# Optimization experiments

Hardware: AMD Instinct MI355X
Metric: run time of the kernel (lower is better)

## Reference

```python
import jax, jax.numpy as jnp
import numpy as np

LEAKY_SLOPE = 0.2   # LeakyReLU alpha from __init__
MASK_VAL = -9.0e15  # same sentinel as torch reference


def setup_inputs() -> dict:
    key = jax.random.key(0)
    k1, k2, k3 = jax.random.split(key, 3)
    B, N, D = 512, 64, 128
    hidden = jax.random.normal(k1, (B, N, D), dtype=jnp.float32)
    adj = jax.random.randint(k2, (B, N, N), 0, 5)  # edge types 0..4
    a = jax.random.normal(k3, (4, D), dtype=jnp.float32) * 0.1  # stacked a_0..a_3
    return {"hidden": hidden, "adj": adj, "a": a}


def reference(hidden, adj, a):
    # e_k[b,i,j] = leakyrelu( sum_d hidden[b,i,d]*hidden[b,j,d]*a[k,d] )
    # Never materializes the [B,N,N,D] tensor: contract (hidden * a_k) @ hidden^T.
    e = jnp.einsum('kd,bid,bjd->kbij', a, hidden, hidden)  # [4,B,N,N]
    e = jnp.where(e >= 0, e, LEAKY_SLOPE * e)
    mask = jnp.full(e.shape[1:], MASK_VAL, dtype=e.dtype)
    alpha = jnp.where(adj == 1, e[0], mask)
    alpha = jnp.where(adj == 2, e[1], alpha)
    alpha = jnp.where(adj == 3, e[2], alpha)
    alpha = jnp.where(adj == 4, e[3], alpha)
    alpha = jax.nn.softmax(alpha, axis=-1)          # [B,N,N]
    return jnp.matmul(alpha, hidden)                # [B,N,D]
```

## Files before the change

### kernel.cpp

```cpp
#include <hip/hip_runtime.h>
#include <hip/hip_bf16.h>


#define NB 512
#define NN 64
#define ND 128
#define HS 136
#define AS 72
#define AJS 65

typedef __bf16 bf16x8 __attribute__((ext_vector_type(8)));
typedef __bf16 bf16x4 __attribute__((ext_vector_type(4)));
typedef float  f32x4  __attribute__((ext_vector_type(4)));

__global__ __launch_bounds__(256)
void gat_kernel(const float* __restrict__ hidden,
                const int*   __restrict__ adj,
                const float* __restrict__ a,
                float*       __restrict__ out)
{
    __shared__ __bf16 h_lds[NN * HS];
    __shared__ __bf16 h_tr[8 * NN * 16];
    __shared__ __bf16 al_lds[NN * AS];
    __shared__ float  a_lds[4 * ND];
    __shared__ int    adj_lds[NN * AJS];

    const int t = threadIdx.x;
    const int l = t & 63;
    const int w = t >> 6;
    const int b = blockIdx.x;
    const int g  = l >> 4;
    const int g8 = g << 3;
    const int i0 = w * 16 + (g << 2);

    const float4* hin = (const float4*)(hidden + (size_t)b * NN * ND);
    #pragma unroll
    for (int it = 0; it < 8; ++it) {
        int row = ((l >> 2) & 15) | ((it >> 1) << 4);
        int f4  = (l & 3) | (w << 2) | ((it & 1) << 4);
        float4 v = hin[row * 32 + f4];
        bf16x4 pk = { (__bf16)v.x, (__bf16)v.y, (__bf16)v.z, (__bf16)v.w };
        int c4 = f4 << 2;
        *(bf16x4*)&h_lds[row * HS + c4] = pk;
        *(bf16x4*)&h_tr[((c4 >> 4) << 10) + (row << 4) + (c4 & 15)] = pk;
    }
    const int4* adjin = (const int4*)(adj + (size_t)b * NN * NN);
    #pragma unroll
    for (int it = 0; it < 4; ++it) {
        int idx = it * 256 + t;
        int4 v = adjin[idx];
        int ri = idx >> 4;
        int c4 = (idx & 15) << 2;
        int* p = &adj_lds[ri * AJS + c4];
        p[0] = v.x; p[1] = v.y; p[2] = v.z; p[3] = v.w;
    }
    a_lds[t]       = a[t];
    a_lds[t + 256] = a[t + 256];
    __syncthreads();

    const int irow = w * 16 + (l & 15);
    f32x4 acc[4][4];
    #pragma unroll
    for (int ct = 0; ct < 4; ++ct)
        #pragma unroll
        for (int k = 0; k < 4; ++k)
            acc[ct][k] = (f32x4){0.f, 0.f, 0.f, 0.f};

    #pragma unroll
    for (int kk = 0; kk < 4; ++kk) {
        int d0 = kk * 32 + g8;
        bf16x8 hf = *(const bf16x8*)&h_lds[irow * HS + d0];
        float hff[8];
        #pragma unroll
        for (int e = 0; e < 8; ++e) hff[e] = (float)hf[e];
        bf16x8 hk[4];
        #pragma unroll
        for (int k = 0; k < 4; ++k) {
            float4 alo = *(const float4*)&a_lds[k * ND + d0];
            float4 ahi = *(const float4*)&a_lds[k * ND + d0 + 4];
            bf16x8 r;
            r[0] = (__bf16)(hff[0] * alo.x); r[1] = (__bf16)(hff[1] * alo.y);
            r[2] = (__bf16)(hff[2] * alo.z); r[3] = (__bf16)(hff[3] * alo.w);
            r[4] = (__bf16)(hff[4] * ahi.x); r[5] = (__bf16)(hff[5] * ahi.y);
            r[6] = (__bf16)(hff[6] * ahi.z); r[7] = (__bf16)(hff[7] * ahi.w);
            hk[k] = r;
        }
        bf16x8 bfr[4];
        #pragma unroll
        for (int ct = 0; ct < 4; ++ct)
            bfr[ct] = *(const bf16x8*)&h_lds[(ct * 16 + (l & 15)) * HS + d0];
        #pragma unroll
        for (int ct = 0; ct < 4; ++ct)
            #pragma unroll
            for (int k = 0; k < 4; ++k)
                acc[ct][k] = __builtin_amdgcn_mfma_f32_16x16x32_bf16(hk[k], bfr[ct], acc[ct][k], 0, 0, 0);
    }

    float sel[4][4];
    #pragma unroll
    for (int ct = 0; ct < 4; ++ct)
        #pragma unroll
        for (int r = 0; r < 4; ++r) {
            int av = adj_lds[(i0 + r) * AJS + ct * 16 + (l & 15)];
            float e0 = fmaxf(acc[ct][0][r], 0.2f * acc[ct][0][r]);
            float e1 = fmaxf(acc[ct][1][r], 0.2f * acc[ct][1][r]);
            float e2 = fmaxf(acc[ct][2][r], 0.2f * acc[ct][2][r]);
            float e3 = fmaxf(acc[ct][3][r], 0.2f * acc[ct][3][r]);
            sel[ct][r] = av == 1 ? e0 : av == 2 ? e1 : av == 3 ? e2 : av == 4 ? e3 : -9.0e15f;
        }

    #pragma unroll
    for (int r = 0; r < 4; ++r) {
        float m = fmaxf(fmaxf(sel[0][r], sel[1][r]), fmaxf(sel[2][r], sel[3][r]));
        m = fmaxf(m, __shfl_xor(m, 1));
        m = fmaxf(m, __shfl_xor(m, 2));
        m = fmaxf(m, __shfl_xor(m, 4));
        m = fmaxf(m, __shfl_xor(m, 8));
        float p0 = __expf(sel[0][r] - m);
        float p1 = __expf(sel[1][r] - m);
        float p2 = __expf(sel[2][r] - m);
        float p3 = __expf(sel[3][r] - m);
        float s = p0 + p1 + p2 + p3;
        s += __shfl_xor(s, 1);
        s += __shfl_xor(s, 2);
        s += __shfl_xor(s, 4);
        s += __shfl_xor(s, 8);
        float inv = 1.0f / s;
        int i = i0 + r;
        al_lds[i * AS +  0 + (l & 15)] = (__bf16)(p0 * inv);
        al_lds[i * AS + 16 + (l & 15)] = (__bf16)(p1 * inv);
        al_lds[i * AS + 32 + (l & 15)] = (__bf16)(p2 * inv);
        al_lds[i * AS + 48 + (l & 15)] = (__bf16)(p3 * inv);
    }

    const int ia = w * 16 + (l & 15);
    bf16x8 pB0 = *(const bf16x8*)&al_lds[ia * AS + g8];
    bf16x8 pB1 = *(const bf16x8*)&al_lds[ia * AS + 32 + g8];
    float* outb = out + (size_t)b * NN * ND;
    unsigned trb = (unsigned)(unsigned long long)(&h_tr[0])
                 + (unsigned)(((l & 15) << 3) + (g << 8));
    #pragma unroll
    for (int dt = 0; dt < 8; ++dt) {
        unsigned ab = trb + dt * 2048;
        bf16x4 r0, r1, r2, r3;
        asm volatile("ds_read_b64_tr_b16 %0, %1"             : "=v"(r0) : "v"(ab));
        asm volatile("ds_read_b64_tr_b16 %0, %1 offset:128"  : "=v"(r1) : "v"(ab));
        asm volatile("ds_read_b64_tr_b16 %0, %1 offset:1024" : "=v"(r2) : "v"(ab));
        asm volatile("ds_read_b64_tr_b16 %0, %1 offset:1152" : "=v"(r3) : "v"(ab));
        asm volatile("s_waitcnt lgkmcnt(0)" ::: "memory");
        __builtin_amdgcn_sched_barrier(0);
        bf16x8 A0 = __builtin_shufflevector(r0, r1, 0, 1, 2, 3, 4, 5, 6, 7);
        bf16x8 A1 = __builtin_shufflevector(r2, r3, 0, 1, 2, 3, 4, 5, 6, 7);
        f32x4 o = {0.f, 0.f, 0.f, 0.f};
        o = __builtin_amdgcn_mfma_f32_16x16x32_bf16(A0, pB0, o, 0, 0, 0);
        o = __builtin_amdgcn_mfma_f32_16x16x32_bf16(A1, pB1, o, 0, 0, 0);
        float4 st = { o[0], o[1], o[2], o[3] };
        *(float4*)&outb[ia * ND + dt * 16 + (g << 2)] = st;
    }
}

extern "C" void kernel_launch(void* const* d_in, const int* in_sizes, int n_in,
                              void* d_out, int out_size, void* d_ws, size_t ws_size,
                              hipStream_t stream) {
    const float* hidden = (const float*)d_in[0];
    const int*   adj    = (const int*)d_in[1];
    const float* a      = (const float*)d_in[2];
    float*       out    = (float*)d_out;
    gat_kernel<<<NB, 256, 0, stream>>>(hidden, adj, a, out);
}
```

Before: 17.12 us.

## Process two batches per block with warp-specialized score/softmax and PV pipeline

Each 512-thread block now handles two batch items. Warps 0-3 compute scores and softmax while warps 4-7 stage the second batch's hidden tile and then run the alpha·V product for the first batch, so the two stages overlap. Adjacency values are loaded straight into registers instead of going through LDS, and softmax normalization is deferred to a per-row reciprocal applied at output. This halves the grid to 256 blocks with one block per CU, which risks lower occupancy and less latency hiding.

```diff
diff --git a/kernel.cpp b/kernel.cpp
--- a/kernel.cpp
+++ b/kernel.cpp
@@ -2,62 +2,21 @@
 #include <hip/hip_bf16.h>
 
 
-#define NB 512
 #define NN 64
 #define ND 128
 #define HS 136
 #define AS 72
-#define AJS 65
 
 typedef __bf16 bf16x8 __attribute__((ext_vector_type(8)));
 typedef __bf16 bf16x4 __attribute__((ext_vector_type(4)));
 typedef float  f32x4  __attribute__((ext_vector_type(4)));
 
-__global__ __launch_bounds__(256)
-void gat_kernel(const float* __restrict__ hidden,
-                const int*   __restrict__ adj,
-                const float* __restrict__ a,
-                float*       __restrict__ out)
+__device__ __forceinline__ void egemm_softmax(
+    const __bf16* __restrict__ h, const float* __restrict__ a_lds,
+    const int (*adjv)[4], __bf16* __restrict__ al, float* __restrict__ invl,
+    int w, int l, int g, int g8)
 {
-    __shared__ __bf16 h_lds[NN * HS];
-    __shared__ __bf16 h_tr[8 * NN * 16];
-    __shared__ __bf16 al_lds[NN * AS];
-    __shared__ float  a_lds[4 * ND];
-    __shared__ int    adj_lds[NN * AJS];
-
-    const int t = threadIdx.x;
-    const int l = t & 63;
-    const int w = t >> 6;
-    const int b = blockIdx.x;
-    const int g  = l >> 4;
-    const int g8 = g << 3;
-    const int i0 = w * 16 + (g << 2);
-
-    const float4* hin = (const float4*)(hidden + (size_t)b * NN * ND);
-    #pragma unroll
-    for (int it = 0; it < 8; ++it) {
-        int row = ((l >> 2) & 15) | ((it >> 1) << 4);
-        int f4  = (l & 3) | (w << 2) | ((it & 1) << 4);
-        float4 v = hin[row * 32 + f4];
-        bf16x4 pk = { (__bf16)v.x, (__bf16)v.y, (__bf16)v.z, (__bf16)v.w };
-        int c4 = f4 << 2;
-        *(bf16x4*)&h_lds[row * HS + c4] = pk;
-        *(bf16x4*)&h_tr[((c4 >> 4) << 10) + (row << 4) + (c4 & 15)] = pk;
-    }
-    const int4* adjin = (const int4*)(adj + (size_t)b * NN * NN);
-    #pragma unroll
-    for (int it = 0; it < 4; ++it) {
-        int idx = it * 256 + t;
-        int4 v = adjin[idx];
-        int ri = idx >> 4;
-        int c4 = (idx & 15) << 2;
-        int* p = &adj_lds[ri * AJS + c4];
-        p[0] = v.x; p[1] = v.y; p[2] = v.z; p[3] = v.w;
-    }
-    a_lds[t]       = a[t];
-    a_lds[t + 256] = a[t + 256];
-    __syncthreads();
-
+    const int i0   = w * 16 + (g << 2);
     const int irow = w * 16 + (l & 15);
     f32x4 acc[4][4];
     #pragma unroll
@@ -69,7 +28,7 @@
     #pragma unroll
     for (int kk = 0; kk < 4; ++kk) {
         int d0 = kk * 32 + g8;
-        bf16x8 hf = *(const bf16x8*)&h_lds[irow * HS + d0];
+        bf16x8 hf = *(const bf16x8*)&h[irow * HS + d0];
         float hff[8];
         #pragma unroll
         for (int e = 0; e < 8; ++e) hff[e] = (float)hf[e];
@@ -88,7 +47,7 @@
         bf16x8 bfr[4];
         #pragma unroll
         for (int ct = 0; ct < 4; ++ct)
-            bfr[ct] = *(const bf16x8*)&h_lds[(ct * 16 + (l & 15)) * HS + d0];
+            bfr[ct] = *(const bf16x8*)&h[(ct * 16 + (l & 15)) * HS + d0];
         #pragma unroll
         for (int ct = 0; ct < 4; ++ct)
             #pragma unroll
@@ -101,7 +60,7 @@
     for (int ct = 0; ct < 4; ++ct)
         #pragma unroll
         for (int r = 0; r < 4; ++r) {
-            int av = adj_lds[(i0 + r) * AJS + ct * 16 + (l & 15)];
+            int av = adjv[ct][r];
             float e0 = fmaxf(acc[ct][0][r], 0.2f * acc[ct][0][r]);
             float e1 = fmaxf(acc[ct][1][r], 0.2f * acc[ct][1][r]);
             float e2 = fmaxf(acc[ct][2][r], 0.2f * acc[ct][2][r]);
@@ -125,22 +84,30 @@
         s += __shfl_xor(s, 2);
         s += __shfl_xor(s, 4);
         s += __shfl_xor(s, 8);
-        float inv = 1.0f / s;
         int i = i0 + r;
-        al_lds[i * AS +  0 + (l & 15)] = (__bf16)(p0 * inv);
-        al_lds[i * AS + 16 + (l & 15)] = (__bf16)(p1 * inv);
-        al_lds[i * AS + 32 + (l & 15)] = (__bf16)(p2 * inv);
-        al_lds[i * AS + 48 + (l & 15)] = (__bf16)(p3 * inv);
-    }
-
-    const int ia = w * 16 + (l & 15);
-    bf16x8 pB0 = *(const bf16x8*)&al_lds[ia * AS + g8];
-    bf16x8 pB1 = *(const bf16x8*)&al_lds[ia * AS + 32 + g8];
-    float* outb = out + (size_t)b * NN * ND;
-    unsigned trb = (unsigned)(unsigned long long)(&h_tr[0])
+        al[i * AS +  0 + (l & 15)] = (__bf16)p0;
+        al[i * AS + 16 + (l & 15)] = (__bf16)p1;
+        al[i * AS + 32 + (l & 15)] = (__bf16)p2;
+        al[i * AS + 48 + (l & 15)] = (__bf16)p3;
+        if ((l & 15) == 0) invl[i] = 1.0f / s;
+    }
+}
+
+template<int NDT>
+__device__ __forceinline__ void pv_phase(
+    const __bf16* __restrict__ htr, const __bf16* __restrict__ al,
+    const float* __restrict__ invl, float* __restrict__ outb,
+    int itile, int dt0, int l, int g, int g8)
+{
+    const int ia = itile * 16 + (l & 15);
+    bf16x8 pB0 = *(const bf16x8*)&al[ia * AS + g8];
+    bf16x8 pB1 = *(const bf16x8*)&al[ia * AS + 32 + g8];
+    float invr = invl[ia];
+    unsigned trb = (unsigned)(unsigned long long)htr
                  + (unsigned)(((l & 15) << 3) + (g << 8));
     #pragma unroll
-    for (int dt = 0; dt < 8; ++dt) {
+    for (int q = 0; q < NDT; ++q) {
+        int dt = dt0 + q;
         unsigned ab = trb + dt * 2048;
         bf16x4 r0, r1, r2, r3;
         asm volatile("ds_read_b64_tr_b16 %0, %1"             : "=v"(r0) : "v"(ab));
@@ -154,9 +121,105 @@
         f32x4 o = {0.f, 0.f, 0.f, 0.f};
         o = __builtin_amdgcn_mfma_f32_16x16x32_bf16(A0, pB0, o, 0, 0, 0);
         o = __builtin_amdgcn_mfma_f32_16x16x32_bf16(A1, pB1, o, 0, 0, 0);
-        float4 st = { o[0], o[1], o[2], o[3] };
+        float4 st = { o[0] * invr, o[1] * invr, o[2] * invr, o[3] * invr };
         *(float4*)&outb[ia * ND + dt * 16 + (g << 2)] = st;
     }
+}
+
+__global__ __launch_bounds__(512, 1)
+void gat_kernel(const float* __restrict__ hidden,
+                const int*   __restrict__ adj,
+                const float* __restrict__ a,
+                float*       __restrict__ out)
+{
+    __shared__ __bf16 h_lds[2][NN * HS];
+    __shared__ __bf16 h_tr[2][8 * NN * 16];
+    __shared__ __bf16 al_lds[2][NN * AS];
+    __shared__ float  inv_lds[2][NN];
+    __shared__ float  a_lds[4 * ND];
+
+    const int t = threadIdx.x;
+    const int l = t & 63;
+    const int w = t >> 6;
+    const int g  = l >> 4;
+    const int g8 = g << 3;
+    const size_t b0 = 2 * (size_t)blockIdx.x;
+    const size_t b1 = b0 + 1;
+
+    const float4* hin0 = (const float4*)(hidden + b0 * NN * ND);
+    const float4* hin1 = (const float4*)(hidden + b1 * NN * ND);
+
+    float4 sv[4];
+    int srow[4], sf4[4];
+    #pragma unroll
+    for (int s = 0; s < 4; ++s) {
+        int cb = (w & 3) | ((s & 1) << 2);
+        int rb = (w >> 2) | ((s >> 1) << 1);
+        srow[s] = ((l >> 2) & 15) | (rb << 4);
+        sf4[s]  = (l & 3) | (cb << 2);
+        sv[s] = hin0[srow[s] * 32 + sf4[s]];
+    }
+    float4 pv[8];
+    int prow[8], pf4[8];
+    if (w >= 4) {
+        #pragma unroll
+        for (int s = 0; s < 8; ++s) {
+            int cb = ((w - 4) & 3) | ((s & 1) << 2);
+            int rb = s >> 1;
+            prow[s] = ((l >> 2) & 15) | (rb << 4);
+            pf4[s]  = (l & 3) | (cb << 2);
+            pv[s] = hin1[prow[s] * 32 + pf4[s]];
+        }
+    }
+    int adjv0[4][4], adjv1[4][4];
+    if (w < 4) {
+        const int i0 = w * 16 + (g << 2);
+        const int* a0 = adj + b0 * NN * NN;
+        const int* a1 = adj + b1 * NN * NN;
+        #pragma unroll
+        for (int ct = 0; ct < 4; ++ct)
+            #pragma unroll
+            for (int r = 0; r < 4; ++r) {
+                adjv0[ct][r] = a0[(i0 + r) * NN + ct * 16 + (l & 15)];
+                adjv1[ct][r] = a1[(i0 + r) * NN + ct * 16 + (l & 15)];
+            }
+    }
+    a_lds[t] = a[t];
+
+    #pragma unroll
+    for (int s = 0; s < 4; ++s) {
+        float4 v = sv[s];
+        bf16x4 pk = { (__bf16)v.x, (__bf16)v.y, (__bf16)v.z, (__bf16)v.w };
+        int c4 = sf4[s] << 2;
+        *(bf16x4*)&h_lds[0][srow[s] * HS + c4] = pk;
+        *(bf16x4*)&h_tr[0][((c4 >> 4) << 10) + (srow[s] << 4) + (c4 & 15)] = pk;
+    }
+    __syncthreads();
+
+    if (w < 4) {
+        egemm_softmax(h_lds[0], a_lds, adjv0, al_lds[0], inv_lds[0], w, l, g, g8);
+    } else {
+        #pragma unroll
+        for (int s = 0; s < 8; ++s) {
+            float4 v = pv[s];
+            bf16x4 pk = { (__bf16)v.x, (__bf16)v.y, (__bf16)v.z, (__bf16)v.w };
+            int c4 = pf4[s] << 2;
+            *(bf16x4*)&h_lds[1][prow[s] * HS + c4] = pk;
+            *(bf16x4*)&h_tr[1][((c4 >> 4) << 10) + (prow[s] << 4) + (c4 & 15)] = pk;
+        }
+    }
+    __syncthreads();
+
+    if (w < 4) {
+        egemm_softmax(h_lds[1], a_lds, adjv1, al_lds[1], inv_lds[1], w, l, g, g8);
+    } else {
+        pv_phase<8>(h_tr[0], al_lds[0], inv_lds[0],
+                    out + b0 * NN * ND, w - 4, 0, l, g, g8);
+    }
+    __syncthreads();
+
+    pv_phase<4>(h_tr[1], al_lds[1], inv_lds[1],
+                out + b1 * NN * ND, w & 3, (w >> 2) * 4, l, g, g8);
 }
 
 extern "C" void kernel_launch(void* const* d_in, const int* in_sizes, int n_in,
@@ -166,5 +229,5 @@
     const int*   adj    = (const int*)d_in[1];
     const float* a      = (const float*)d_in[2];
     float*       out    = (float*)d_out;
-    gat_kernel<<<NB, 256, 0, stream>>>(hidden, adj, a, out);
-}
+    gat_kernel<<<256, 512, 0, stream>>>(hidden, adj, a, out);
+}
```

Result: slower. 21.88 us (+27.8%).
